# Performance work log

Hardware: AMD Instinct MI355X
Metric: run time of the kernel (lower is better)

The kernel has to match this reference:

```python
import jax, jax.numpy as jnp
import numpy as np

B, T, D_BERT, D_LSTM, N_CLASS, X = 32, 512, 768, 256, 16, 10
H2 = D_LSTM // 2  # per-direction hidden size


def setup_inputs() -> dict:
    key = jax.random.key(0)
    ks = jax.random.split(key, 24)
    rn = lambda k, s: jax.random.normal(k, s, jnp.float32) * 0.05
    return {
        "x": jax.random.normal(ks[0], (B, T, D_BERT), jnp.float32),
        "mask": jnp.ones((B, T), jnp.int32),
        # encoder BiLSTM (PyTorch gate order i,f,g,o)
        "Wih_f": rn(ks[1], (4 * H2, D_BERT)), "Whh_f": rn(ks[2], (4 * H2, H2)),
        "bih_f": rn(ks[3], (4 * H2,)), "bhh_f": rn(ks[4], (4 * H2,)),
        "Wih_r": rn(ks[5], (4 * H2, D_BERT)), "Whh_r": rn(ks[6], (4 * H2, H2)),
        "bih_r": rn(ks[7], (4 * H2,)), "bhh_r": rn(ks[8], (4 * H2,)),
        # attention projections
        "fc1_w": rn(ks[9], (X, 2 * D_LSTM)),
        "fc2_w": rn(ks[10], (1, X)),
        "fc3_w": rn(ks[11], (D_LSTM, 2 * D_LSTM)), "fc3_b": rn(ks[12], (D_LSTM,)),
        # decoder LSTMCell + output linear
        "Wih_d": rn(ks[13], (4 * D_LSTM, D_LSTM + N_CLASS)),
        "Whh_d": rn(ks[14], (4 * D_LSTM, D_LSTM)),
        "bih_d": rn(ks[15], (4 * D_LSTM,)), "bhh_d": rn(ks[16], (4 * D_LSTM,)),
        "lin_w": rn(ks[17], (N_CLASS, D_LSTM)), "lin_b": rn(ks[18], (N_CLASS,)),
    }


def _cell(xt, h, c, Wih, Whh, bih, bhh):
    g = xt @ Wih.T + bih + h @ Whh.T + bhh
    i, f, gg, o = jnp.split(g, 4, axis=-1)
    c = jax.nn.sigmoid(f) * c + jax.nn.sigmoid(i) * jnp.tanh(gg)
    h = jax.nn.sigmoid(o) * jnp.tanh(c)
    return h, c


def _lstm(x_tbd, Wih, Whh, bih, bhh):
    # x_tbd: [T, B, D] -> hs [T, B, H]
    Bn, H = x_tbd.shape[1], Whh.shape[1]
    def step(carry, xt):
        h, c = _cell(xt, carry[0], carry[1], Wih, Whh, bih, bhh)
        return (h, c), h
    z = jnp.zeros((Bn, H), x_tbd.dtype)
    _, hs = jax.lax.scan(step, (z, z), x_tbd)
    return hs


def _forward(x, mask, Wih_f, Whh_f, bih_f, bhh_f, Wih_r, Whh_r, bih_r, bhh_r,
             fc1_w, fc2_w, fc3_w, fc3_b, Wih_d, Whh_d, bih_d, bhh_d, lin_w, lin_b):
    xt = x.transpose(1, 0, 2)  # [T,B,D_BERT]
    hf = _lstm(xt, Wih_f, Whh_f, bih_f, bhh_f)
    hr = _lstm(xt[::-1], Wih_r, Whh_r, bih_r, bhh_r)[::-1]
    hs = jnp.concatenate([hf, hr], -1).transpose(1, 0, 2)  # [B,T,D_LSTM]

    # additive attention: fc1(cat(query,key)) == query@Wq.T + key@Wk.T
    Wq, Wk = fc1_w[:, :D_LSTM], fc1_w[:, D_LSTM:]
    qp = hs @ Wq.T  # [B,T,X]
    kp = hs @ Wk.T  # [B,T,X]
    a = jnp.tanh(qp[:, :, None, :] + kp[:, None, :, :]) @ fc2_w[0]  # [B,T,T]
    m = jnp.where(mask == 0, -jnp.inf, 0.0)[:, None, :]  # [B,1,T]
    w = jax.nn.softmax(a + m, axis=-1)
    ctx = jnp.einsum('bij,bjd->bid', w, hs)  # [B,T,D_LSTM]
    y_enc = jnp.concatenate([hs, ctx], -1) @ fc3_w.T + fc3_b  # [B,T,D_LSTM]

    init_h = hs[:, -1, :]
    def dstep(carry, xt_):
        h, c, y = carry
        h, c = _cell(jnp.concatenate([xt_, y], -1), h, c, Wih_d, Whh_d, bih_d, bhh_d)
        y = jax.nn.softmax(h @ lin_w.T + lin_b, axis=-1)
        return (h, c, y), y
    init = (init_h, jnp.zeros_like(init_h), jnp.zeros((x.shape[0], N_CLASS), x.dtype))
    _, ys = jax.lax.scan(dstep, init, y_enc.transpose(1, 0, 2))
    return ys.transpose(1, 0, 2)  # [B,T,N_CLASS]


def reference(x, mask, Wih_f, Whh_f, bih_f, bhh_f, Wih_r, Whh_r, bih_r, bhh_r,
              fc1_w, fc2_w, fc3_w, fc3_b, Wih_d, Whh_d, bih_d, bhh_d, lin_w, lin_b):
    return _forward(x, mask, Wih_f, Whh_f, bih_f, bhh_f, Wih_r, Whh_r, bih_r, bhh_r,
                    fc1_w, fc2_w, fc3_w, fc3_b, Wih_d, Whh_d, bih_d, bhh_d, lin_w, lin_b)
```

## Files before the change

kernel.cpp:

```cpp
#include <hip/hip_runtime.h>

#define TSEQ 512
#define NB   32
#define DB   768
#define H2E  128
#define DL   256
#define NC   16

typedef unsigned long long ull;
typedef float f32x4 __attribute__((ext_vector_type(4)));
typedef short bf16x8 __attribute__((ext_vector_type(8)));
typedef unsigned short u16x8 __attribute__((ext_vector_type(8)));

__device__ __forceinline__ float sigf(float x) { return 1.0f / (1.0f + __expf(-x)); }
__device__ __forceinline__ float tanhfast(float x) { return 1.0f - 2.0f / (1.0f + __expf(2.0f * x)); }

__device__ __forceinline__ void cvt_split(float a, unsigned short& hi, unsigned short& lo) {
    unsigned u = __float_as_uint(a);
    unsigned h = (u + 0x7FFFu + ((u >> 16) & 1u)) >> 16;
    float hf = __uint_as_float(h << 16);
    float d = a - hf;
    unsigned ud = __float_as_uint(d);
    unsigned l = (ud + 0x7FFFu + ((ud >> 16) & 1u)) >> 16;
    hi = (unsigned short)h;
    lo = (unsigned short)l;
}

#define LDST 40
template <int MODE>
__global__ __launch_bounds__(256) void gemm_mfma(
    const float* __restrict__ A, int lda,
    const float* __restrict__ W, int ldw,
    const float* __restrict__ b1, const float* __restrict__ b2,
    float* __restrict__ C, int ldc, int K)
{
    __shared__ unsigned short Ah[128][LDST];
    __shared__ unsigned short Al[128][LDST];
    __shared__ unsigned short Wh[128][LDST];
    __shared__ unsigned short Wl[128][LDST];

    const int tid = threadIdx.x;
    const int m0 = blockIdx.x * 128;
    const int n0 = blockIdx.y * 128;
    const int wave = tid >> 6, lane = tid & 63;
    const int wr = wave >> 1, wc = wave & 1;
    const int fr = lane & 15;
    const int fq = lane >> 4;
    const int srow = tid >> 1, skoff = (tid & 1) * 16;

    f32x4 acc[4][4] = {};

    for (int k0 = 0; k0 < K; k0 += 32) {
        __syncthreads();
        {
            const float* src = A + (size_t)(m0 + srow) * lda + k0 + skoff;
            u16x8 vh0, vh1, vl0, vl1;
#pragma unroll
            for (int e = 0; e < 8; ++e) {
                unsigned short h, l;
                cvt_split(src[e], h, l);
                vh0[e] = h; vl0[e] = l;
                cvt_split(src[e + 8], h, l);
                vh1[e] = h; vl1[e] = l;
            }
            *(u16x8*)&Ah[srow][skoff]     = vh0;
            *(u16x8*)&Ah[srow][skoff + 8] = vh1;
            *(u16x8*)&Al[srow][skoff]     = vl0;
            *(u16x8*)&Al[srow][skoff + 8] = vl1;
        }
        {
            const float* src = W + (size_t)(n0 + srow) * ldw + k0 + skoff;
            u16x8 vh0, vh1, vl0, vl1;
#pragma unroll
            for (int e = 0; e < 8; ++e) {
                unsigned short h, l;
                cvt_split(src[e], h, l);
                vh0[e] = h; vl0[e] = l;
                cvt_split(src[e + 8], h, l);
                vh1[e] = h; vl1[e] = l;
            }
            *(u16x8*)&Wh[srow][skoff]     = vh0;
            *(u16x8*)&Wh[srow][skoff + 8] = vh1;
            *(u16x8*)&Wl[srow][skoff]     = vl0;
            *(u16x8*)&Wl[srow][skoff + 8] = vl1;
        }
        __syncthreads();

        bf16x8 ah[4], al[4], bh[4], bl[4];
#pragma unroll
        for (int i = 0; i < 4; ++i) {
            const int r = wr * 64 + i * 16 + fr;
            ah[i] = *(const bf16x8*)&Ah[r][fq * 8];
            al[i] = *(const bf16x8*)&Al[r][fq * 8];
        }
#pragma unroll
        for (int j = 0; j < 4; ++j) {
            const int r = wc * 64 + j * 16 + fr;
            bh[j] = *(const bf16x8*)&Wh[r][fq * 8];
            bl[j] = *(const bf16x8*)&Wl[r][fq * 8];
        }
#pragma unroll
        for (int i = 0; i < 4; ++i)
#pragma unroll
            for (int j = 0; j < 4; ++j) {
                acc[i][j] = __builtin_amdgcn_mfma_f32_16x16x32_bf16(ah[i], bh[j], acc[i][j], 0, 0, 0);
                acc[i][j] = __builtin_amdgcn_mfma_f32_16x16x32_bf16(ah[i], bl[j], acc[i][j], 0, 0, 0);
                acc[i][j] = __builtin_amdgcn_mfma_f32_16x16x32_bf16(al[i], bh[j], acc[i][j], 0, 0, 0);
            }
    }

#pragma unroll
    for (int i = 0; i < 4; ++i) {
#pragma unroll
        for (int r = 0; r < 4; ++r) {
            int gm = m0 + wr * 64 + i * 16 + fq * 4 + r;
            int orow;
            if (MODE == 0) orow = gm;
            else {
                int bb = gm >> 9;
                int tt = gm & (TSEQ - 1);
                orow = (MODE == 1 ? tt : (TSEQ - 1 - tt)) * NB + bb;
            }
            float* crow = C + (size_t)orow * ldc;
#pragma unroll
            for (int j = 0; j < 4; ++j) {
                int gn = n0 + wc * 64 + j * 16 + fr;
                float bias = (b1 ? b1[gn] : 0.f) + (b2 ? b2[gn] : 0.f);
                crow[gn] = acc[i][j][r] + bias;
            }
        }
    }
}

template <int MODE>
__global__ __launch_bounds__(256) void gemm_nt(
    const float* __restrict__ A, int lda,
    const float* __restrict__ W, int ldw,
    const float* __restrict__ b1, const float* __restrict__ b2,
    float* __restrict__ C, int ldc, int N, int K)
{
    __shared__ float As[16][68];
    __shared__ float Ws[16][68];
    const int tid = threadIdx.x;
    const int m0 = blockIdx.x * 64;
    const int n0 = blockIdx.y * 64;
    const int tx = tid & 15, ty = tid >> 4;
    const int lrow = tid >> 2;
    const int lk = (tid & 3) * 4;
    float acc[4][4] = {};

    for (int k0 = 0; k0 < K; k0 += 16) {
        float4 av = *(const float4*)(A + (size_t)(m0 + lrow) * lda + k0 + lk);
        float4 wv = make_float4(0.f, 0.f, 0.f, 0.f);
        if (n0 + lrow < N)
            wv = *(const float4*)(W + (size_t)(n0 + lrow) * ldw + k0 + lk);
        As[lk + 0][lrow] = av.x; As[lk + 1][lrow] = av.y;
        As[lk + 2][lrow] = av.z; As[lk + 3][lrow] = av.w;
        Ws[lk + 0][lrow] = wv.x; Ws[lk + 1][lrow] = wv.y;
        Ws[lk + 2][lrow] = wv.z; Ws[lk + 3][lrow] = wv.w;
        __syncthreads();
#pragma unroll
        for (int kk = 0; kk < 16; ++kk) {
            float a0 = As[kk][ty * 4 + 0], a1 = As[kk][ty * 4 + 1];
            float a2 = As[kk][ty * 4 + 2], a3 = As[kk][ty * 4 + 3];
            float w0 = Ws[kk][tx * 4 + 0], w1 = Ws[kk][tx * 4 + 1];
            float w2 = Ws[kk][tx * 4 + 2], w3 = Ws[kk][tx * 4 + 3];
            acc[0][0] += a0 * w0; acc[0][1] += a0 * w1; acc[0][2] += a0 * w2; acc[0][3] += a0 * w3;
            acc[1][0] += a1 * w0; acc[1][1] += a1 * w1; acc[1][2] += a1 * w2; acc[1][3] += a1 * w3;
            acc[2][0] += a2 * w0; acc[2][1] += a2 * w1; acc[2][2] += a2 * w2; acc[2][3] += a2 * w3;
            acc[3][0] += a3 * w0; acc[3][1] += a3 * w1; acc[3][2] += a3 * w2; acc[3][3] += a3 * w3;
        }
        __syncthreads();
    }

#pragma unroll
    for (int i = 0; i < 4; ++i) {
        int gm = m0 + ty * 4 + i;
        int orow;
        if (MODE == 0) orow = gm;
        else {
            int bb = gm >> 9;
            int tt = gm & (TSEQ - 1);
            orow = (MODE == 1 ? tt : (TSEQ - 1 - tt)) * NB + bb;
        }
#pragma unroll
        for (int j = 0; j < 4; ++j) {
            int gn = n0 + tx * 4 + j;
            if (gn < N) {
                float bias = (b1 ? b1[gn] : 0.f) + (b2 ? b2[gn] : 0.f);
                C[(size_t)orow * ldc + gn] = acc[i][j] + bias;
            }
        }
    }
}

__global__ __launch_bounds__(512) void enc_scan(
    const float* __restrict__ Gf, const float* __restrict__ Gr,
    const float* __restrict__ Whh_f, const float* __restrict__ Whh_r,
    float* __restrict__ hs_ctx)
{
    const int dir = blockIdx.x & 1;
    const int b = blockIdx.x >> 1;
    const float* __restrict__ G = dir ? Gr : Gf;
    const float* __restrict__ Whh = dir ? Whh_r : Whh_f;
    const int j = threadIdx.x;

    __shared__ float4 h4[H2E / 4];
    __shared__ float gates[4 * H2E];
    float* h_s = (float*)h4;

    float4 w[32];
#pragma unroll
    for (int k = 0; k < 32; ++k)
        w[k] = *(const float4*)(Whh + (size_t)j * H2E + k * 4);

    float c = 0.f;
    if (j < H2E) h_s[j] = 0.f;
    __syncthreads();

    for (int t = 0; t < TSEQ; ++t) {
        const float* grow = G + ((size_t)t * NB + b) * 512;
        float acc = grow[j];
#pragma unroll
        for (int k = 0; k < 32; ++k) {
            float4 hv = h4[k];
            acc += w[k].x * hv.x + w[k].y * hv.y + w[k].z * hv.z + w[k].w * hv.w;
        }
        gates[j] = acc;
        __syncthreads();
        if (j < H2E) {
            float ig = sigf(gates[j]);
            float fg = sigf(gates[j + H2E]);
            float gg = tanhfast(gates[j + 2 * H2E]);
            float og = sigf(gates[j + 3 * H2E]);
            c = fg * c + ig * gg;
            float h = og * tanhfast(c);
            h_s[j] = h;
            int tout = dir ? (TSEQ - 1 - t) : t;
            hs_ctx[((size_t)b * TSEQ + tout) * 512 + dir * H2E + j] = h;
        }
        __syncthreads();
    }
}

__global__ __launch_bounds__(256) void attn_w(
    const float* __restrict__ qp, const float* __restrict__ kp,
    const int* __restrict__ mask, const float* __restrict__ fc2,
    float* __restrict__ wout)
{
    const int bi = blockIdx.x;
    const int b = bi >> 9;
    const int tid = threadIdx.x;
    __shared__ float kps[TSEQ * 11];
    __shared__ float red[8];

    const float* kpb = kp + (size_t)b * TSEQ * 10;
    for (int idx = tid; idx < TSEQ * 10; idx += 256) {
        int j = idx / 10, xx = idx - j * 10;
        kps[j * 11 + xx] = kpb[idx];
    }
    float q[10], vv[10];
#pragma unroll
    for (int xx = 0; xx < 10; ++xx) {
        q[xx] = qp[(size_t)bi * 10 + xx];
        vv[xx] = fc2[xx];
    }
    __syncthreads();

    float a[2];
#pragma unroll
    for (int jj = 0; jj < 2; ++jj) {
        int j = tid + jj * 256;
        float s = 0.f;
#pragma unroll
        for (int xx = 0; xx < 10; ++xx)
            s += vv[xx] * tanhfast(q[xx] + kps[j * 11 + xx]);
        if (mask[(size_t)b * TSEQ + j] == 0) s = -1e30f;
        a[jj] = s;
    }

    float m = fmaxf(a[0], a[1]);
#pragma unroll
    for (int o = 32; o >= 1; o >>= 1) m = fmaxf(m, __shfl_xor(m, o));
    if ((tid & 63) == 0) red[tid >> 6] = m;
    __syncthreads();
    m = fmaxf(fmaxf(red[0], red[1]), fmaxf(red[2], red[3]));

    float e0 = __expf(a[0] - m), e1 = __expf(a[1] - m);
    float s = e0 + e1;
#pragma unroll
    for (int o = 32; o >= 1; o >>= 1) s += __shfl_xor(s, o);
    if ((tid & 63) == 0) red[4 + (tid >> 6)] = s;
    __syncthreads();
    s = (red[4] + red[5]) + (red[6] + red[7]);
    float inv = 1.0f / s;
    wout[(size_t)bi * TSEQ + tid] = e0 * inv;
    wout[(size_t)bi * TSEQ + tid + 256] = e1 * inv;
}

__global__ __launch_bounds__(256) void bgemm_nn(
    const float* __restrict__ Wmat,
    float* __restrict__ hs_ctx)
{
    __shared__ float As[16][68];
    __shared__ float Bs[16][68];
    const int tid = threadIdx.x;
    const int b = blockIdx.z;
    const int i0 = blockIdx.x * 64;
    const int d0 = blockIdx.y * 64;
    const int tx = tid & 15, ty = tid >> 4;
    float acc[4][4] = {};
    const float* Ab = Wmat + (size_t)b * TSEQ * TSEQ;
    const float* Bb = hs_ctx + (size_t)b * TSEQ * 512;

    for (int k0 = 0; k0 < TSEQ; k0 += 16) {
        {
            int r = tid >> 2, kq = (tid & 3) * 4;
            float4 v = *(const float4*)(Ab + (size_t)(i0 + r) * TSEQ + k0 + kq);
            As[kq + 0][r] = v.x; As[kq + 1][r] = v.y; As[kq + 2][r] = v.z; As[kq + 3][r] = v.w;
        }
        {
            int kk = tid >> 4, dq = (tid & 15) * 4;
            float4 v = *(const float4*)(Bb + (size_t)(k0 + kk) * 512 + d0 + dq);
            *(float4*)&Bs[kk][dq] = v;
        }
        __syncthreads();
#pragma unroll
        for (int kk = 0; kk < 16; ++kk) {
            float a0 = As[kk][ty * 4 + 0], a1 = As[kk][ty * 4 + 1];
            float a2 = As[kk][ty * 4 + 2], a3 = As[kk][ty * 4 + 3];
            float b0 = Bs[kk][tx * 4 + 0], b1 = Bs[kk][tx * 4 + 1];
            float b2 = Bs[kk][tx * 4 + 2], b3 = Bs[kk][tx * 4 + 3];
            acc[0][0] += a0 * b0; acc[0][1] += a0 * b1; acc[0][2] += a0 * b2; acc[0][3] += a0 * b3;
            acc[1][0] += a1 * b0; acc[1][1] += a1 * b1; acc[1][2] += a1 * b2; acc[1][3] += a1 * b3;
            acc[2][0] += a2 * b0; acc[2][1] += a2 * b1; acc[2][2] += a2 * b2; acc[2][3] += a2 * b3;
            acc[3][0] += a3 * b0; acc[3][1] += a3 * b1; acc[3][2] += a3 * b2; acc[3][3] += a3 * b3;
        }
        __syncthreads();
    }
#pragma unroll
    for (int i = 0; i < 4; ++i)
#pragma unroll
        for (int j = 0; j < 4; ++j)
            hs_ctx[((size_t)b * TSEQ + i0 + ty * 4 + i) * 512 + 256 + d0 + tx * 4 + j] = acc[i][j];
}

__global__ __launch_bounds__(256) void dec_init4(
    const float* __restrict__ hs_ctx, ull* hbuf, ull* lbuf)
{
    const int gid = blockIdx.x * 256 + threadIdx.x;
    for (int idx = gid; idx < 32768; idx += 16 * 256) {
        ull v = 0ull;
        if (idx < 8192) {
            int b = idx >> 8, u = idx & 255;
            float hv = hs_ctx[((size_t)b * TSEQ + (TSEQ - 1)) * 512 + u];
            v = (1ull << 32) | (ull)__float_as_uint(hv);
        }
        ull* dst = (idx < 16384) ? (hbuf + idx) : (lbuf + (idx - 16384));
        __hip_atomic_store(dst, v, __ATOMIC_RELAXED, __HIP_MEMORY_SCOPE_AGENT);
    }
}

__global__ __launch_bounds__(256) void dec_scan9(
    const float* __restrict__ Gd,
    const float* __restrict__ Whh,
    const float* __restrict__ Wih,
    const float* __restrict__ lin_w,
    const float* __restrict__ lin_b,
    ull* hbuf,
    ull* lbuf,
    float* __restrict__ out)
{
    const int tid = threadIdx.x;
    const int rg  = blockIdx.x & 15;
    const int bg  = blockIdx.x >> 4;
    const int wave = tid >> 6;
    const int lane = tid & 63;
    const int fr = lane & 15;
    const int fq = lane >> 4;
    const bool isw1 = (wave == 1);
    const int ybb = (tid >> 4) & 3;
    const int ycls = tid & 15;

    __shared__ unsigned short wbh[64][264];
    __shared__ unsigned short wbl[64][264];
    __shared__ unsigned short hbh[4][264];
    __shared__ unsigned short hbl[4][264];
    __shared__ float gpart[4][4][18];
    __shared__ float ylds[4][17];
    __shared__ float hnew[4][17];
    __shared__ float linl[16][17];
    __shared__ float wylds[64][17];

    for (int idx = tid; idx < 64 * 256; idx += 256) {
        int row = idx >> 8, c = idx & 255;
        int j = ((row >> 4) << 8) + rg * 16 + (row & 15);
        unsigned short h, l;
        cvt_split(Whh[(size_t)j * 256 + c], h, l);
        wbh[row][c] = h;
        wbl[row][c] = l;
    }
    {
        int r = tid >> 2, c0 = (tid & 3) * 4;
        int j = ((r >> 4) << 8) + rg * 16 + (r & 15);
        const float* src = Wih + (size_t)j * 272 + 256 + c0;
        wylds[r][c0 + 0] = src[0]; wylds[r][c0 + 1] = src[1];
        wylds[r][c0 + 2] = src[2]; wylds[r][c0 + 3] = src[3];
    }
    linl[tid >> 4][tid & 15] = lin_w[(tid >> 4) * 256 + rg * 16 + (tid & 15)];
    const float lb = lin_b[ycls];
    float cstate = 0.f;
    __syncthreads();

    for (int t = 0; t <= TSEQ; ++t) {
        const unsigned want = (unsigned)(t + 1);
        const ull* hsrc = hbuf + (size_t)(t & 1) * 8192 + (size_t)bg * 1024;
        const ull* lsrc = lbuf + (size_t)(t & 1) * 8192 + (size_t)bg * 1024;

        float gdv[4] = {0.f, 0.f, 0.f, 0.f};
        if (tid < 64 && t < TSEQ) {
            const float* gb = Gd + ((size_t)t * NB + bg * 4 + ybb) * 1024 + rg * 16 + ycls;
#pragma unroll
            for (int q = 0; q < 4; ++q) gdv[q] = gb[q * 256];
        }
        __builtin_amdgcn_sched_barrier(0);

        if (isw1) {
            float yv = 0.f;
            if (t > 0) {
                float lsum;
                for (;;) {
                    lsum = lb;
                    bool ok = true;
#pragma unroll
                    for (int r = 0; r < 16; ++r) {
                        ull lv = __hip_atomic_load(lsrc + ybb * 256 + r * 16 + ycls,
                                                   __ATOMIC_RELAXED, __HIP_MEMORY_SCOPE_AGENT);
                        ok &= ((unsigned)(lv >> 32) == want);
                        lsum += __uint_as_float((unsigned)lv);
                    }
                    if (ok) break;
                    __builtin_amdgcn_s_sleep(1);
                }
                float m = lsum;
#pragma unroll
                for (int o = 1; o < 16; o <<= 1) m = fmaxf(m, __shfl_xor(m, o, 16));
                float e = __expf(lsum - m);
                float ss = e;
#pragma unroll
                for (int o = 1; o < 16; o <<= 1) ss += __shfl_xor(ss, o, 16);
                yv = e / ss;
                if (rg == 0)
                    out[(((size_t)(bg * 4 + ybb)) * TSEQ + (t - 1)) * NC + ycls] = yv;
            }
            ylds[ybb][ycls] = yv;
        }

        {
            ull h0, h1, h2, h3;
            for (;;) {
                h0 = __hip_atomic_load(hsrc + tid,       __ATOMIC_RELAXED, __HIP_MEMORY_SCOPE_AGENT);
                h1 = __hip_atomic_load(hsrc + tid + 256, __ATOMIC_RELAXED, __HIP_MEMORY_SCOPE_AGENT);
                h2 = __hip_atomic_load(hsrc + tid + 512, __ATOMIC_RELAXED, __HIP_MEMORY_SCOPE_AGENT);
                h3 = __hip_atomic_load(hsrc + tid + 768, __ATOMIC_RELAXED, __HIP_MEMORY_SCOPE_AGENT);
                if (((unsigned)(h0 >> 32) == want) && ((unsigned)(h1 >> 32) == want) &&
                    ((unsigned)(h2 >> 32) == want) && ((unsigned)(h3 >> 32) == want))
                    break;
                __builtin_amdgcn_s_sleep(1);
            }
            unsigned short hh, hl;
            cvt_split(__uint_as_float((unsigned)h0), hh, hl);
            hbh[0][tid] = hh; hbl[0][tid] = hl;
            cvt_split(__uint_as_float((unsigned)h1), hh, hl);
            hbh[1][tid] = hh; hbl[1][tid] = hl;
            cvt_split(__uint_as_float((unsigned)h2), hh, hl);
            hbh[2][tid] = hh; hbl[2][tid] = hl;
            cvt_split(__uint_as_float((unsigned)h3), hh, hl);
            hbh[3][tid] = hh; hbl[3][tid] = hl;
        }
        __syncthreads();

        if (t == TSEQ) break;

        {
            f32x4 acc = {};
            const int abrow = lane & 3;
            const int wrow = wave * 16 + fr;
#pragma unroll
            for (int ks = 0; ks < 8; ++ks) {
                const int kc = ks * 32 + fq * 8;
                bf16x8 ahi = *(const bf16x8*)&hbh[abrow][kc];
                bf16x8 alo = *(const bf16x8*)&hbl[abrow][kc];
                bf16x8 bhi = *(const bf16x8*)&wbh[wrow][kc];
                bf16x8 blo = *(const bf16x8*)&wbl[wrow][kc];
                acc = __builtin_amdgcn_mfma_f32_16x16x32_bf16(ahi, bhi, acc, 0, 0, 0);
                acc = __builtin_amdgcn_mfma_f32_16x16x32_bf16(ahi, blo, acc, 0, 0, 0);
                acc = __builtin_amdgcn_mfma_f32_16x16x32_bf16(alo, bhi, acc, 0, 0, 0);
            }
            if (fq == 0) {
#pragma unroll
                for (int reg = 0; reg < 4; ++reg)
                    gpart[wave][reg][fr] = acc[reg];
            }
        }
        __syncthreads();

        if (tid < 64) {
            const int bb = ybb, u = ycls;
            float g[4];
#pragma unroll
            for (int q = 0; q < 4; ++q) {
                float s = gpart[q][bb][u] + gdv[q];
                const int r = q * 16 + u;
#pragma unroll
                for (int c = 0; c < 16; ++c)
                    s += wylds[r][c] * ylds[bb][c];
                g[q] = s;
            }
            float ig = sigf(g[0]), fg = sigf(g[1]);
            float gv = tanhfast(g[2]), og = sigf(g[3]);
            cstate = fg * cstate + ig * gv;
            float h = og * tanhfast(cstate);
            hnew[bb][u] = h;
            const ull tagbits = ((ull)(unsigned)(t + 2)) << 32;
            const size_t oidx = (size_t)((t + 1) & 1) * 8192
                              + (size_t)(bg * 4 + bb) * 256 + rg * 16 + u;
            __hip_atomic_store(hbuf + oidx, tagbits | (ull)__float_as_uint(h),
                               __ATOMIC_RELAXED, __HIP_MEMORY_SCOPE_AGENT);
            float lp = 0.f;
#pragma unroll
            for (int u2 = 0; u2 < 16; ++u2)
                lp += linl[u][u2] * hnew[bb][u2];
            __hip_atomic_store(lbuf + oidx, tagbits | (ull)__float_as_uint(lp),
                               __ATOMIC_RELAXED, __HIP_MEMORY_SCOPE_AGENT);
        }
    }
}

extern "C" void kernel_launch(void* const* d_in, const int* in_sizes, int n_in,
                              void* d_out, int out_size, void* d_ws, size_t ws_size,
                              hipStream_t stream)
{
    const float* x     = (const float*)d_in[0];
    const int*   mask  = (const int*)d_in[1];
    const float* Wih_f = (const float*)d_in[2];
    const float* Whh_f = (const float*)d_in[3];
    const float* bih_f = (const float*)d_in[4];
    const float* bhh_f = (const float*)d_in[5];
    const float* Wih_r = (const float*)d_in[6];
    const float* Whh_r = (const float*)d_in[7];
    const float* bih_r = (const float*)d_in[8];
    const float* bhh_r = (const float*)d_in[9];
    const float* fc1_w = (const float*)d_in[10];
    const float* fc2_w = (const float*)d_in[11];
    const float* fc3_w = (const float*)d_in[12];
    const float* fc3_b = (const float*)d_in[13];
    const float* Wih_d = (const float*)d_in[14];
    const float* Whh_d = (const float*)d_in[15];
    const float* bih_d = (const float*)d_in[16];
    const float* bhh_d = (const float*)d_in[17];
    const float* lin_w = (const float*)d_in[18];
    const float* lin_b = (const float*)d_in[19];

    float* ws = (float*)d_ws;
    float* Gf   = ws;
    float* Gr   = ws + 8388608;
    float* hs   = ws + 16777216;
    float* wat  = ws + 25165824;
    float* qp   = ws + 33554432;
    float* kp   = ws + 33718272;
    float* Gd   = ws;
    float* yenc = wat;
    ull* hbuf = (ull*)(wat + 4194304);
    ull* lbuf = hbuf + 16384;

    float* outp = (float*)d_out;
    const int M = NB * TSEQ;
    dim3 blk(256);

    gemm_mfma<1><<<dim3(M / 128, 4), blk, 0, stream>>>(x, DB, Wih_f, DB, bih_f, bhh_f, Gf, 512, DB);
    gemm_mfma<2><<<dim3(M / 128, 4), blk, 0, stream>>>(x, DB, Wih_r, DB, bih_r, bhh_r, Gr, 512, DB);
    enc_scan<<<dim3(64), dim3(512), 0, stream>>>(Gf, Gr, Whh_f, Whh_r, hs);
    gemm_nt<0><<<dim3(M / 64, 1), blk, 0, stream>>>(hs, 512, fc1_w, 512, nullptr, nullptr, qp, 10, 10, 256);
    gemm_nt<0><<<dim3(M / 64, 1), blk, 0, stream>>>(hs, 512, fc1_w + 256, 512, nullptr, nullptr, kp, 10, 10, 256);
    attn_w<<<dim3(M), blk, 0, stream>>>(qp, kp, mask, fc2_w, wat);
    bgemm_nn<<<dim3(8, 4, NB), blk, 0, stream>>>(wat, hs);
    gemm_mfma<0><<<dim3(M / 128, 2), blk, 0, stream>>>(hs, 512, fc3_w, 512, fc3_b, nullptr, yenc, 256, 512);
    dec_init4<<<dim3(16), blk, 0, stream>>>(hs, hbuf, lbuf);
    gemm_mfma<1><<<dim3(M / 128, 8), blk, 0, stream>>>(yenc, 256, Wih_d, 272, bih_d, bhh_d, Gd, 1024, 256);
    dec_scan9<<<dim3(128), blk, 0, stream>>>(Gd, Whh_d, Wih_d, lin_w, lin_b, hbuf, lbuf, outp);
}
```

Measured before the change: 2.761 ms.

## Compute decoder logits redundantly per block to drop the second cross-block exchange

```diff
diff --git a/kernel.cpp b/kernel.cpp
--- a/kernel.cpp
+++ b/kernel.cpp
@@ -345,54 +345,52 @@
             hs_ctx[((size_t)b * TSEQ + i0 + ty * 4 + i) * 512 + 256 + d0 + tx * 4 + j] = acc[i][j];
 }
 
-__global__ __launch_bounds__(256) void dec_init4(
-    const float* __restrict__ hs_ctx, ull* hbuf, ull* lbuf)
+__global__ __launch_bounds__(256) void dec_init5(
+    const float* __restrict__ hs_ctx, ull* hbuf)
 {
     const int gid = blockIdx.x * 256 + threadIdx.x;
-    for (int idx = gid; idx < 32768; idx += 16 * 256) {
+    for (int idx = gid; idx < 16384; idx += 16 * 256) {
         ull v = 0ull;
         if (idx < 8192) {
             int b = idx >> 8, u = idx & 255;
             float hv = hs_ctx[((size_t)b * TSEQ + (TSEQ - 1)) * 512 + u];
             v = (1ull << 32) | (ull)__float_as_uint(hv);
         }
-        ull* dst = (idx < 16384) ? (hbuf + idx) : (lbuf + (idx - 16384));
-        __hip_atomic_store(dst, v, __ATOMIC_RELAXED, __HIP_MEMORY_SCOPE_AGENT);
-    }
-}
-
-__global__ __launch_bounds__(256) void dec_scan9(
+        __hip_atomic_store(hbuf + idx, v, __ATOMIC_RELAXED, __HIP_MEMORY_SCOPE_AGENT);
+    }
+}
+
+__global__ __launch_bounds__(320) void dec_scan10(
     const float* __restrict__ Gd,
     const float* __restrict__ Whh,
     const float* __restrict__ Wih,
     const float* __restrict__ lin_w,
     const float* __restrict__ lin_b,
     ull* hbuf,
-    ull* lbuf,
     float* __restrict__ out)
 {
     const int tid = threadIdx.x;
     const int rg  = blockIdx.x & 15;
     const int bg  = blockIdx.x >> 4;
-    const int wave = tid >> 6;
+    const int wave = tid / 64;
     const int lane = tid & 63;
     const int fr = lane & 15;
     const int fq = lane >> 4;
-    const bool isw1 = (wave == 1);
-    const int ybb = (tid >> 4) & 3;
-    const int ycls = tid & 15;
+    const bool isw4 = (wave == 4);
+    const int ybb = (lane >> 4) & 3;
+    const int ycls = lane & 15;
 
     __shared__ unsigned short wbh[64][264];
     __shared__ unsigned short wbl[64][264];
+    __shared__ unsigned short lwh[16][264];
+    __shared__ unsigned short lwl[16][264];
     __shared__ unsigned short hbh[4][264];
     __shared__ unsigned short hbl[4][264];
     __shared__ float gpart[4][4][18];
-    __shared__ float ylds[4][17];
-    __shared__ float hnew[4][17];
-    __shared__ float linl[16][17];
+    __shared__ float lgp[4][18];
     __shared__ float wylds[64][17];
 
-    for (int idx = tid; idx < 64 * 256; idx += 256) {
+    for (int idx = tid; idx < 64 * 256; idx += 320) {
         int row = idx >> 8, c = idx & 255;
         int j = ((row >> 4) << 8) + rg * 16 + (row & 15);
         unsigned short h, l;
@@ -400,14 +398,18 @@
         wbh[row][c] = h;
         wbl[row][c] = l;
     }
-    {
-        int r = tid >> 2, c0 = (tid & 3) * 4;
+    for (int idx = tid; idx < 16 * 256; idx += 320) {
+        int row = idx >> 8, c = idx & 255;
+        unsigned short h, l;
+        cvt_split(lin_w[(size_t)row * 256 + c], h, l);
+        lwh[row][c] = h;
+        lwl[row][c] = l;
+    }
+    for (int idx = tid; idx < 64 * 16; idx += 320) {
+        int r = idx >> 4, c = idx & 15;
         int j = ((r >> 4) << 8) + rg * 16 + (r & 15);
-        const float* src = Wih + (size_t)j * 272 + 256 + c0;
-        wylds[r][c0 + 0] = src[0]; wylds[r][c0 + 1] = src[1];
-        wylds[r][c0 + 2] = src[2]; wylds[r][c0 + 3] = src[3];
-    }
-    linl[tid >> 4][tid & 15] = lin_w[(tid >> 4) * 256 + rg * 16 + (tid & 15)];
+        wylds[r][c] = Wih[(size_t)j * 272 + 256 + c];
+    }
     const float lb = lin_b[ycls];
     float cstate = 0.f;
     __syncthreads();
@@ -415,48 +417,16 @@
     for (int t = 0; t <= TSEQ; ++t) {
         const unsigned want = (unsigned)(t + 1);
         const ull* hsrc = hbuf + (size_t)(t & 1) * 8192 + (size_t)bg * 1024;
-        const ull* lsrc = lbuf + (size_t)(t & 1) * 8192 + (size_t)bg * 1024;
 
         float gdv[4] = {0.f, 0.f, 0.f, 0.f};
-        if (tid < 64 && t < TSEQ) {
+        if (isw4 && t < TSEQ) {
             const float* gb = Gd + ((size_t)t * NB + bg * 4 + ybb) * 1024 + rg * 16 + ycls;
 #pragma unroll
             for (int q = 0; q < 4; ++q) gdv[q] = gb[q * 256];
         }
         __builtin_amdgcn_sched_barrier(0);
 
-        if (isw1) {
-            float yv = 0.f;
-            if (t > 0) {
-                float lsum;
-                for (;;) {
-                    lsum = lb;
-                    bool ok = true;
-#pragma unroll
-                    for (int r = 0; r < 16; ++r) {
-                        ull lv = __hip_atomic_load(lsrc + ybb * 256 + r * 16 + ycls,
-                                                   __ATOMIC_RELAXED, __HIP_MEMORY_SCOPE_AGENT);
-                        ok &= ((unsigned)(lv >> 32) == want);
-                        lsum += __uint_as_float((unsigned)lv);
-                    }
-                    if (ok) break;
-                    __builtin_amdgcn_s_sleep(1);
-                }
-                float m = lsum;
-#pragma unroll
-                for (int o = 1; o < 16; o <<= 1) m = fmaxf(m, __shfl_xor(m, o, 16));
-                float e = __expf(lsum - m);
-                float ss = e;
-#pragma unroll
-                for (int o = 1; o < 16; o <<= 1) ss += __shfl_xor(ss, o, 16);
-                yv = e / ss;
-                if (rg == 0)
-                    out[(((size_t)(bg * 4 + ybb)) * TSEQ + (t - 1)) * NC + ycls] = yv;
-            }
-            ylds[ybb][ycls] = yv;
-        }
-
-        {
+        if (tid < 256) {
             ull h0, h1, h2, h3;
             for (;;) {
                 h0 = __hip_atomic_load(hsrc + tid,       __ATOMIC_RELAXED, __HIP_MEMORY_SCOPE_AGENT);
@@ -480,60 +450,74 @@
         }
         __syncthreads();
 
-        if (t == TSEQ) break;
-
         {
-            f32x4 acc = {};
+            f32x4 acc1 = {}, acc2 = {};
             const int abrow = lane & 3;
-            const int wrow = wave * 16 + fr;
+            const unsigned short* browh = isw4 ? &lwh[fr][0] : &wbh[wave * 16 + fr][0];
+            const unsigned short* browl = isw4 ? &lwl[fr][0] : &wbl[wave * 16 + fr][0];
 #pragma unroll
             for (int ks = 0; ks < 8; ++ks) {
                 const int kc = ks * 32 + fq * 8;
                 bf16x8 ahi = *(const bf16x8*)&hbh[abrow][kc];
                 bf16x8 alo = *(const bf16x8*)&hbl[abrow][kc];
-                bf16x8 bhi = *(const bf16x8*)&wbh[wrow][kc];
-                bf16x8 blo = *(const bf16x8*)&wbl[wrow][kc];
-                acc = __builtin_amdgcn_mfma_f32_16x16x32_bf16(ahi, bhi, acc, 0, 0, 0);
-                acc = __builtin_amdgcn_mfma_f32_16x16x32_bf16(ahi, blo, acc, 0, 0, 0);
-                acc = __builtin_amdgcn_mfma_f32_16x16x32_bf16(alo, bhi, acc, 0, 0, 0);
+                bf16x8 bhi = *(const bf16x8*)&browh[kc];
+                bf16x8 blo = *(const bf16x8*)&browl[kc];
+                acc1 = __builtin_amdgcn_mfma_f32_16x16x32_bf16(ahi, bhi, acc1, 0, 0, 0);
+                acc2 = __builtin_amdgcn_mfma_f32_16x16x32_bf16(ahi, blo, acc2, 0, 0, 0);
+                acc2 = __builtin_amdgcn_mfma_f32_16x16x32_bf16(alo, bhi, acc2, 0, 0, 0);
             }
             if (fq == 0) {
 #pragma unroll
-                for (int reg = 0; reg < 4; ++reg)
-                    gpart[wave][reg][fr] = acc[reg];
-            }
-        }
-        __syncthreads();
-
-        if (tid < 64) {
+                for (int reg = 0; reg < 4; ++reg) {
+                    float v = acc1[reg] + acc2[reg];
+                    if (isw4) lgp[reg][fr] = v;
+                    else      gpart[wave][reg][fr] = v;
+                }
+            }
+        }
+        __syncthreads();
+
+        if (isw4) {
             const int bb = ybb, u = ycls;
-            float g[4];
-#pragma unroll
-            for (int q = 0; q < 4; ++q) {
-                float s = gpart[q][bb][u] + gdv[q];
-                const int r = q * 16 + u;
-#pragma unroll
-                for (int c = 0; c < 16; ++c)
-                    s += wylds[r][c] * ylds[bb][c];
-                g[q] = s;
-            }
-            float ig = sigf(g[0]), fg = sigf(g[1]);
-            float gv = tanhfast(g[2]), og = sigf(g[3]);
-            cstate = fg * cstate + ig * gv;
-            float h = og * tanhfast(cstate);
-            hnew[bb][u] = h;
-            const ull tagbits = ((ull)(unsigned)(t + 2)) << 32;
-            const size_t oidx = (size_t)((t + 1) & 1) * 8192
-                              + (size_t)(bg * 4 + bb) * 256 + rg * 16 + u;
-            __hip_atomic_store(hbuf + oidx, tagbits | (ull)__float_as_uint(h),
-                               __ATOMIC_RELAXED, __HIP_MEMORY_SCOPE_AGENT);
-            float lp = 0.f;
-#pragma unroll
-            for (int u2 = 0; u2 < 16; ++u2)
-                lp += linl[u][u2] * hnew[bb][u2];
-            __hip_atomic_store(lbuf + oidx, tagbits | (ull)__float_as_uint(lp),
-                               __ATOMIC_RELAXED, __HIP_MEMORY_SCOPE_AGENT);
-        }
+            float yv = 0.f;
+            if (t > 0) {
+                float lv = lgp[bb][u] + lb;
+                float m = lv;
+#pragma unroll
+                for (int o = 1; o < 16; o <<= 1) m = fmaxf(m, __shfl_xor(m, o, 16));
+                float e = __expf(lv - m);
+                float ss = e;
+#pragma unroll
+                for (int o = 1; o < 16; o <<= 1) ss += __shfl_xor(ss, o, 16);
+                yv = e / ss;
+                if (rg == 0)
+                    out[(((size_t)(bg * 4 + bb)) * TSEQ + (t - 1)) * NC + u] = yv;
+            }
+            if (t < TSEQ) {
+                float g[4];
+#pragma unroll
+                for (int q = 0; q < 4; ++q) {
+                    float s = gpart[q][bb][u] + gdv[q];
+                    const int r = q * 16 + u;
+#pragma unroll
+                    for (int c = 0; c < 16; ++c) {
+                        float yc = __shfl(yv, (lane & 48) | c);
+                        s += wylds[r][c] * yc;
+                    }
+                    g[q] = s;
+                }
+                float ig = sigf(g[0]), fg = sigf(g[1]);
+                float gv = tanhfast(g[2]), og = sigf(g[3]);
+                cstate = fg * cstate + ig * gv;
+                float h = og * tanhfast(cstate);
+                const ull tagbits = ((ull)(unsigned)(t + 2)) << 32;
+                const size_t oidx = (size_t)((t + 1) & 1) * 8192
+                                  + (size_t)(bg * 4 + bb) * 256 + rg * 16 + u;
+                __hip_atomic_store(hbuf + oidx, tagbits | (ull)__float_as_uint(h),
+                                   __ATOMIC_RELAXED, __HIP_MEMORY_SCOPE_AGENT);
+            }
+        }
+        if (t == TSEQ) break;
     }
 }
 
@@ -572,7 +556,6 @@
     float* Gd   = ws;
     float* yenc = wat;
     ull* hbuf = (ull*)(wat + 4194304);
-    ull* lbuf = hbuf + 16384;
 
     float* outp = (float*)d_out;
     const int M = NB * TSEQ;
@@ -586,7 +569,7 @@
     attn_w<<<dim3(M), blk, 0, stream>>>(qp, kp, mask, fc2_w, wat);
     bgemm_nn<<<dim3(8, 4, NB), blk, 0, stream>>>(wat, hs);
     gemm_mfma<0><<<dim3(M / 128, 2), blk, 0, stream>>>(hs, 512, fc3_w, 512, fc3_b, nullptr, yenc, 256, 512);
-    dec_init4<<<dim3(16), blk, 0, stream>>>(hs, hbuf, lbuf);
+    dec_init5<<<dim3(16), blk, 0, stream>>>(hs, hbuf);
     gemm_mfma<1><<<dim3(M / 128, 8), blk, 0, stream>>>(yenc, 256, Wih_d, 272, bih_d, bhh_d, Gd, 1024, 256);
-    dec_scan9<<<dim3(128), blk, 0, stream>>>(Gd, Whh_d, Wih_d, lin_w, lin_b, hbuf, lbuf, outp);
-}
+    dec_scan10<<<dim3(128), dim3(320), 0, stream>>>(Gd, Whh_d, Wih_d, lin_w, lin_b, hbuf, outp);
+}
```

Result: faster. 2.434 ms (-11.8%).
